# Kernel optimization log

Measured on AMD Instinct MI355X. Metric: run time of the kernel, lower is better.

The kernel has to match this reference:

```python
import jax, jax.numpy as jnp
import numpy as np

EPS = 1e-10

def setup_inputs() -> dict:
    key = jax.random.key(0)
    k1, k2 = jax.random.split(key)
    support_set = jax.random.normal(k1, (8192, 1024), dtype=jnp.float32)
    input_image = jax.random.normal(k2, (2048, 1024), dtype=jnp.float32)
    return {"support_set": support_set, "input_image": input_image}

def reference(support_set, input_image):
    # support_set: [n, d], input_image: [b, d]
    # Faithful to original: input magnitude is a single scalar over the whole
    # [b, d] input matrix; support magnitude is a scalar per support vector.
    input_mag = jax.lax.rsqrt(jnp.maximum(jnp.sum(input_image * input_image), EPS))  # scalar
    support_mag = jax.lax.rsqrt(jnp.maximum(jnp.sum(support_set * support_set, axis=1), EPS))  # [n]
    dot = jnp.einsum('bd,nd->nb', input_image, support_set)  # [n, b]
    sims = dot * support_mag[:, None] * input_mag  # [n, b]
    return sims[:, :, None]  # [n, b, 1] == torch.stack(...)[n,b,1].squeeze(1) (no-op for b>1)
```

## Files before the change

kernel.cpp:

```cpp
#include <hip/hip_runtime.h>
#include <hip/hip_bf16.h>
#include <stdint.h>
#include <stddef.h>

#define M_DIM 8192
#define N_DIM 2048
#define K_DIM 1024

#define BM 256
#define BN 256
#define BK 64
#define NKT (K_DIM / BK)
#define NITER (NKT / 2)

typedef __attribute__((ext_vector_type(8))) short short8;
typedef __attribute__((ext_vector_type(4))) float float4v;

static __device__ __forceinline__ unsigned short f2bf(float x) {
  union { float f; unsigned u; } c; c.f = x;
  return (unsigned short)((c.u + 0x7FFFu + ((c.u >> 16) & 1u)) >> 16);
}

#define GLOAD_LDS16(g, l)                                           \
  __builtin_amdgcn_global_load_lds(                                 \
      (const __attribute__((address_space(1))) void*)(g),           \
      (__attribute__((address_space(3))) void*)(l), 16, 0, 0)

__global__ __launch_bounds__(256) void prep(
    const float* __restrict__ S, const float* __restrict__ I,
    unsigned short* __restrict__ Sb, unsigned short* __restrict__ Ib,
    float* __restrict__ smag, float* __restrict__ partials) {
  const int t = threadIdx.x;
  const int lane = t & 63;
  const int wave = t >> 6;
  const int blk = blockIdx.x;
  const bool isS = blk < 2048;
  const int row = (isS ? blk : blk - 2048) * 4 + wave;
  const float* src = (isS ? S : I) + (size_t)row * K_DIM;
  unsigned short* dst = (isS ? Sb : Ib) + (size_t)row * K_DIM;

  float ss = 0.f;
#pragma unroll
  for (int i = 0; i < 4; ++i) {
    const float4 v = reinterpret_cast<const float4*>(src)[lane + i * 64];
    ushort4 b;
    b.x = f2bf(v.x); b.y = f2bf(v.y); b.z = f2bf(v.z); b.w = f2bf(v.w);
    reinterpret_cast<ushort4*>(dst)[lane + i * 64] = b;
    ss += v.x * v.x + v.y * v.y + v.z * v.z + v.w * v.w;
  }
#pragma unroll
  for (int m = 32; m >= 1; m >>= 1) ss += __shfl_xor(ss, m, 64);
  if (lane == 0) {
    if (isS) smag[row] = rsqrtf(fmaxf(ss, 1e-10f));
    else     partials[row] = ss;
  }
}

__global__ __launch_bounds__(512, 2) void gemm_bt(
    const unsigned short* __restrict__ A,
    const unsigned short* __restrict__ B,
    const float* __restrict__ smag,
    const float* __restrict__ partials,
    float* __restrict__ C) {
  __shared__ __align__(16) unsigned short lA[32768];
  __shared__ __align__(16) unsigned short lB[32768];
  __shared__ float wsum[8];

  const int t = threadIdx.x;
  const int lane = t & 63;
  const int wave = t >> 6;
  const int wr = wave >> 2;
  const int wc = wave & 3;

  const int blk = blockIdx.x;
  const int xcd = blk & 7;
  const int slot = blk >> 3;
  const int bm = (xcd * 4 + (slot & 3)) * BM;
  const int bn = (slot >> 2) * BN;

  {
    float p = partials[t] + partials[t + 512] + partials[t + 1024] + partials[t + 1536];
#pragma unroll
    for (int m = 32; m >= 1; m >>= 1) p += __shfl_xor(p, m, 64);
    if (lane == 0) wsum[wave] = p;
  }
  asm volatile("s_waitcnt vmcnt(0)" ::: "memory");

  const int srow = t >> 3;
  const int skc = (t & 7) ^ (srow & 7);
  const unsigned short* gA[4];
  const unsigned short* gB[4];
  int aoff[4];
#pragma unroll
  for (int j = 0; j < 4; ++j) {
    gA[j] = A + (size_t)(bm + j * 64 + srow) * K_DIM + skc * 8;
    gB[j] = B + (size_t)(bn + j * 64 + srow) * K_DIM + skc * 8;
    aoff[j] = (j >> 1) * 8192 + (j & 1) * 4096 + wave * 512;
  }

#define STAGE_A(j, buf) do { GLOAD_LDS16(gA[j], &lA[(buf) * 16384 + aoff[j]]); gA[j] += BK; } while (0)
#define STAGE_B(j, buf) do { GLOAD_LDS16(gB[j], &lB[(buf) * 16384 + aoff[j]]); gB[j] += BK; } while (0)
#define SP1(buf) do { STAGE_B(0, buf); STAGE_B(1, buf); } while (0)
#define SP2(buf) do { STAGE_B(2, buf); STAGE_B(3, buf); } while (0)
#define SP3(buf) do { STAGE_A(0, buf); STAGE_A(2, buf); } while (0)
#define SP4(buf) do { STAGE_A(1, buf); STAGE_A(3, buf); } while (0)

  const int fr = lane & 15;
  const int q = lane >> 4;
  const int pc0 = (q ^ (fr & 7)) * 8;
  const int pc1 = ((4 + q) ^ (fr & 7)) * 8;
  const unsigned short* rA = lA + wr * 8192 + fr * 64;
  const unsigned short* rB = lB + (wc >> 1) * 8192 + ((wc & 1) * 64 + fr) * 64;

  short8 af0[2][2], af1[2][2];
  short8 bfA[4][2], bfB[4][2];
  float4v acc[8][4];
#pragma unroll
  for (int i = 0; i < 8; ++i)
#pragma unroll
    for (int j = 0; j < 4; ++j) acc[i][j] = (float4v)0.0f;

#define BARRIER() __builtin_amdgcn_s_barrier()
#define VMW(n) asm volatile("s_waitcnt vmcnt(" #n ")" ::: "memory")
#define PRIO1() __builtin_amdgcn_s_setprio(1)
#define PRIO0() __builtin_amdgcn_s_setprio(0)

#define LOADB(bank, buf) do {                                                  \
    _Pragma("unroll") for (int nj = 0; nj < 4; ++nj) {                         \
      bank[nj][0] = *reinterpret_cast<const short8*>(rB + (buf) * 16384 + nj * 1024 + pc0); \
      bank[nj][1] = *reinterpret_cast<const short8*>(rB + (buf) * 16384 + nj * 1024 + pc1); \
    } } while (0)

#define LOADA(bank, buf, pi) do {                                              \
    _Pragma("unroll") for (int m2 = 0; m2 < 2; ++m2) {                         \
      bank[m2][0] = *reinterpret_cast<const short8*>(rA + (buf) * 16384 + ((pi) * 2 + m2) * 1024 + pc0); \
      bank[m2][1] = *reinterpret_cast<const short8*>(rA + (buf) * 16384 + ((pi) * 2 + m2) * 1024 + pc1); \
    } } while (0)

#define MFMA16(pi, abank, bbank) do {                                          \
    _Pragma("unroll") for (int m2 = 0; m2 < 2; ++m2)                           \
    _Pragma("unroll") for (int nj = 0; nj < 4; ++nj) {                         \
      acc[(pi) * 2 + m2][nj] = __builtin_amdgcn_mfma_f32_16x16x32_bf16(        \
          abank[m2][0], bbank[nj][0], acc[(pi) * 2 + m2][nj], 0, 0, 0);        \
      acc[(pi) * 2 + m2][nj] = __builtin_amdgcn_mfma_f32_16x16x32_bf16(        \
          abank[m2][1], bbank[nj][1], acc[(pi) * 2 + m2][nj], 0, 0, 0);        \
    } } while (0)

#define ITER_F() do {                                                          \
     SP4(1);           BARRIER(); LOADA(af1, 0, 1);                   \
              PRIO1(); MFMA16(0, af0, bfA); PRIO0();                           \
     SP1(0); VMW(10);  BARRIER(); LOADA(af0, 0, 2);                   \
              PRIO1(); MFMA16(1, af1, bfA); PRIO0();                           \
     SP2(0);           BARRIER(); LOADA(af1, 0, 3);                   \
              PRIO1(); MFMA16(2, af0, bfA); PRIO0();                           \
     SP3(0); VMW(8);   BARRIER(); LOADB(bfB, 1); LOADA(af0, 1, 0);    \
              PRIO1(); MFMA16(3, af1, bfA); PRIO0();                           \
     SP4(0);           BARRIER(); LOADA(af1, 1, 1);                   \
              PRIO1(); MFMA16(0, af0, bfB); PRIO0();                           \
     SP1(1); VMW(10);  BARRIER(); LOADA(af0, 1, 2);                   \
              PRIO1(); MFMA16(1, af1, bfB); PRIO0();                           \
     SP2(1);           BARRIER(); LOADA(af1, 1, 3);                   \
              PRIO1(); MFMA16(2, af0, bfB); PRIO0();                           \
     SP3(1); VMW(8);   BARRIER(); LOADB(bfA, 0); LOADA(af0, 0, 0);    \
              PRIO1(); MFMA16(3, af1, bfB); PRIO0();                           \
  } while (0)

#define ITER_T() do {                                                          \
     SP4(1);           BARRIER(); LOADA(af1, 0, 1);                   \
              PRIO1(); MFMA16(0, af0, bfA); PRIO0();                           \
     VMW(8);           BARRIER(); LOADA(af0, 0, 2);                   \
              PRIO1(); MFMA16(1, af1, bfA); PRIO0();                           \
                       BARRIER(); LOADA(af1, 0, 3);                   \
              PRIO1(); MFMA16(2, af0, bfA); PRIO0();                           \
     VMW(2);           BARRIER(); LOADB(bfB, 1); LOADA(af0, 1, 0);    \
              PRIO1(); MFMA16(3, af1, bfA); PRIO0();                           \
                       BARRIER(); LOADA(af1, 1, 1);                   \
              PRIO1(); MFMA16(0, af0, bfB); PRIO0();                           \
     VMW(0);           BARRIER(); LOADA(af0, 1, 2);                   \
              PRIO1(); MFMA16(1, af1, bfB); PRIO0();                           \
                       BARRIER(); LOADA(af1, 1, 3);                   \
              PRIO1(); MFMA16(2, af0, bfB); PRIO0();                           \
                       BARRIER();                                     \
              PRIO1(); MFMA16(3, af1, bfB); PRIO0();                           \
  } while (0)

  SP1(0); SP2(0); SP3(0); SP4(0);
  SP1(1); SP2(1); SP3(1);
  VMW(6);
  BARRIER();
  LOADB(bfA, 0); LOADA(af0, 0, 0);

#pragma unroll 1
  for (int it = 0; it < NITER - 1; ++it) ITER_F();
  ITER_T();

  const float imag = rsqrtf(fmaxf(wsum[0] + wsum[1] + wsum[2] + wsum[3] +
                                  wsum[4] + wsum[5] + wsum[6] + wsum[7], 1e-10f));
#pragma unroll
  for (int mi = 0; mi < 8; ++mi) {
    const int rbase = bm + wr * 128 + mi * 16 + q * 4;
#pragma unroll
    for (int r = 0; r < 4; ++r) {
      const int row = rbase + r;
      const float sc = smag[row] * imag;
      float* crow = C + (size_t)row * N_DIM + bn + wc * 64 + fr;
#pragma unroll
      for (int nj = 0; nj < 4; ++nj) crow[nj * 16] = acc[mi][nj][r] * sc;
    }
  }
}

extern "C" void kernel_launch(void* const* d_in, const int* in_sizes, int n_in,
                              void* d_out, int out_size, void* d_ws, size_t ws_size,
                              hipStream_t stream) {
  const float* S = (const float*)d_in[0];
  const float* I = (const float*)d_in[1];
  float* out = (float*)d_out;

  unsigned char* ws = (unsigned char*)d_ws;
  unsigned short* Sb = (unsigned short*)ws;
  unsigned short* Ib = (unsigned short*)(ws + (size_t)M_DIM * K_DIM * 2);
  float* smag = (float*)(ws + (size_t)M_DIM * K_DIM * 2 + (size_t)N_DIM * K_DIM * 2);
  float* partials = smag + M_DIM;

  hipLaunchKernelGGL(prep, dim3(2560), dim3(256), 0, stream,
                     S, I, Sb, Ib, smag, partials);
  hipLaunchKernelGGL(gemm_bt, dim3((M_DIM / BM) * (N_DIM / BN)), dim3(512), 0, stream,
                     Sb, Ib, smag, partials, out);
}
```

Measured before the change: 126.9 us.

## Restructure GEMM main loop into k-split quarter-step pipeline with nontemporal stores

```diff
diff --git a/kernel.cpp b/kernel.cpp
--- a/kernel.cpp
+++ b/kernel.cpp
@@ -112,8 +112,8 @@
   const unsigned short* rA = lA + wr * 8192 + fr * 64;
   const unsigned short* rB = lB + (wc >> 1) * 8192 + ((wc & 1) * 64 + fr) * 64;
 
-  short8 af0[2][2], af1[2][2];
-  short8 bfA[4][2], bfB[4][2];
+  short8 afA[4], afB[4];
+  short8 bf0[4], bf1[4];
   float4v acc[8][4];
 #pragma unroll
   for (int i = 0; i < 8; ++i)
@@ -125,74 +125,53 @@
 #define PRIO1() __builtin_amdgcn_s_setprio(1)
 #define PRIO0() __builtin_amdgcn_s_setprio(0)
 
-#define LOADB(bank, buf) do {                                                  \
-    _Pragma("unroll") for (int nj = 0; nj < 4; ++nj) {                         \
-      bank[nj][0] = *reinterpret_cast<const short8*>(rB + (buf) * 16384 + nj * 1024 + pc0); \
-      bank[nj][1] = *reinterpret_cast<const short8*>(rB + (buf) * 16384 + nj * 1024 + pc1); \
-    } } while (0)
-
-#define LOADA(bank, buf, pi) do {                                              \
-    _Pragma("unroll") for (int m2 = 0; m2 < 2; ++m2) {                         \
-      bank[m2][0] = *reinterpret_cast<const short8*>(rA + (buf) * 16384 + ((pi) * 2 + m2) * 1024 + pc0); \
-      bank[m2][1] = *reinterpret_cast<const short8*>(rA + (buf) * 16384 + ((pi) * 2 + m2) * 1024 + pc1); \
-    } } while (0)
-
-#define MFMA16(pi, abank, bbank) do {                                          \
-    _Pragma("unroll") for (int m2 = 0; m2 < 2; ++m2)                           \
-    _Pragma("unroll") for (int nj = 0; nj < 4; ++nj) {                         \
-      acc[(pi) * 2 + m2][nj] = __builtin_amdgcn_mfma_f32_16x16x32_bf16(        \
-          abank[m2][0], bbank[nj][0], acc[(pi) * 2 + m2][nj], 0, 0, 0);        \
-      acc[(pi) * 2 + m2][nj] = __builtin_amdgcn_mfma_f32_16x16x32_bf16(        \
-          abank[m2][1], bbank[nj][1], acc[(pi) * 2 + m2][nj], 0, 0, 0);        \
-    } } while (0)
-
-#define ITER_F() do {                                                          \
-     SP4(1);           BARRIER(); LOADA(af1, 0, 1);                   \
-              PRIO1(); MFMA16(0, af0, bfA); PRIO0();                           \
-     SP1(0); VMW(10);  BARRIER(); LOADA(af0, 0, 2);                   \
-              PRIO1(); MFMA16(1, af1, bfA); PRIO0();                           \
-     SP2(0);           BARRIER(); LOADA(af1, 0, 3);                   \
-              PRIO1(); MFMA16(2, af0, bfA); PRIO0();                           \
-     SP3(0); VMW(8);   BARRIER(); LOADB(bfB, 1); LOADA(af0, 1, 0);    \
-              PRIO1(); MFMA16(3, af1, bfA); PRIO0();                           \
-     SP4(0);           BARRIER(); LOADA(af1, 1, 1);                   \
-              PRIO1(); MFMA16(0, af0, bfB); PRIO0();                           \
-     SP1(1); VMW(10);  BARRIER(); LOADA(af0, 1, 2);                   \
-              PRIO1(); MFMA16(1, af1, bfB); PRIO0();                           \
-     SP2(1);           BARRIER(); LOADA(af1, 1, 3);                   \
-              PRIO1(); MFMA16(2, af0, bfB); PRIO0();                           \
-     SP3(1); VMW(8);   BARRIER(); LOADB(bfA, 0); LOADA(af0, 0, 0);    \
-              PRIO1(); MFMA16(3, af1, bfB); PRIO0();                           \
+#define LA(bank, buf, half, s) do {                                            \
+    _Pragma("unroll") for (int m = 0; m < 4; ++m)                              \
+      bank[m] = *reinterpret_cast<const short8*>(                              \
+          rA + (buf) * 16384 + ((half) * 4 + m) * 1024 + ((s) ? pc1 : pc0));   \
   } while (0)
 
-#define ITER_T() do {                                                          \
-     SP4(1);           BARRIER(); LOADA(af1, 0, 1);                   \
-              PRIO1(); MFMA16(0, af0, bfA); PRIO0();                           \
-     VMW(8);           BARRIER(); LOADA(af0, 0, 2);                   \
-              PRIO1(); MFMA16(1, af1, bfA); PRIO0();                           \
-                       BARRIER(); LOADA(af1, 0, 3);                   \
-              PRIO1(); MFMA16(2, af0, bfA); PRIO0();                           \
-     VMW(2);           BARRIER(); LOADB(bfB, 1); LOADA(af0, 1, 0);    \
-              PRIO1(); MFMA16(3, af1, bfA); PRIO0();                           \
-                       BARRIER(); LOADA(af1, 1, 1);                   \
-              PRIO1(); MFMA16(0, af0, bfB); PRIO0();                           \
-     VMW(0);           BARRIER(); LOADA(af0, 1, 2);                   \
-              PRIO1(); MFMA16(1, af1, bfB); PRIO0();                           \
-                       BARRIER(); LOADA(af1, 1, 3);                   \
-              PRIO1(); MFMA16(2, af0, bfB); PRIO0();                           \
-                       BARRIER();                                     \
-              PRIO1(); MFMA16(3, af1, bfB); PRIO0();                           \
+#define LB2(bank, buf, s, j0) do {                                             \
+    _Pragma("unroll") for (int n = 0; n < 2; ++n)                              \
+      bank[(j0) + n] = *reinterpret_cast<const short8*>(                       \
+          rB + (buf) * 16384 + ((j0) + n) * 1024 + ((s) ? pc1 : pc0));         \
   } while (0)
 
+#define MQ(half, abank, bbank) do {                                            \
+    PRIO1();                                                                   \
+    _Pragma("unroll") for (int m = 0; m < 4; ++m)                              \
+    _Pragma("unroll") for (int n = 0; n < 4; ++n)                              \
+      acc[(half) * 4 + m][n] = __builtin_amdgcn_mfma_f32_16x16x32_bf16(        \
+          abank[m], bbank[n], acc[(half) * 4 + m][n], 0, 0, 0);                \
+    PRIO0();                                                                   \
+  } while (0)
+
   SP1(0); SP2(0); SP3(0); SP4(0);
-  SP1(1); SP2(1); SP3(1);
-  VMW(6);
+  SP1(1);
+  VMW(2);
   BARRIER();
-  LOADB(bfA, 0); LOADA(af0, 0, 0);
+  LB2(bf0, 0, 0, 0); LB2(bf0, 0, 0, 2);
+  LA(afA, 0, 0, 0);
 
 #pragma unroll 1
-  for (int it = 0; it < NITER - 1; ++it) ITER_F();
-  ITER_T();
+  for (int it = 0; it < NITER - 1; ++it) {
+     SP2(1); VMW(4); BARRIER(); LA(afB, 0, 1, 0); LB2(bf1, 0, 1, 0); MQ(0, afA, bf0);
+     SP3(1); VMW(4); BARRIER(); LA(afA, 0, 0, 1); LB2(bf1, 0, 1, 2); MQ(1, afB, bf0);
+     SP4(1); VMW(4); BARRIER(); LA(afB, 0, 1, 1); LB2(bf0, 1, 0, 0); MQ(0, afA, bf1);
+     SP1(0); VMW(4); BARRIER(); LA(afA, 1, 0, 0); LB2(bf0, 1, 0, 2); MQ(1, afB, bf1);
+     SP2(0); VMW(4); BARRIER(); LA(afB, 1, 1, 0); LB2(bf1, 1, 1, 0); MQ(0, afA, bf0);
+     SP3(0); VMW(4); BARRIER(); LA(afA, 1, 0, 1); LB2(bf1, 1, 1, 2); MQ(1, afB, bf0);
+     SP4(0); VMW(4); BARRIER(); LA(afB, 1, 1, 1); LB2(bf0, 0, 0, 0); MQ(0, afA, bf1);
+     SP1(1); VMW(4); BARRIER(); LA(afA, 0, 0, 0); LB2(bf0, 0, 0, 2); MQ(1, afB, bf1);
+  }
+   SP2(1); VMW(4); BARRIER(); LA(afB, 0, 1, 0); LB2(bf1, 0, 1, 0); MQ(0, afA, bf0);
+   SP3(1); VMW(4); BARRIER(); LA(afA, 0, 0, 1); LB2(bf1, 0, 1, 2); MQ(1, afB, bf0);
+   SP4(1); VMW(4); BARRIER(); LA(afB, 0, 1, 1); LB2(bf0, 1, 0, 0); MQ(0, afA, bf1);
+           VMW(2); BARRIER(); LA(afA, 1, 0, 0); LB2(bf0, 1, 0, 2); MQ(1, afB, bf1);
+           VMW(0); BARRIER(); LA(afB, 1, 1, 0); LB2(bf1, 1, 1, 0); MQ(0, afA, bf0);
+                   BARRIER(); LA(afA, 1, 0, 1); LB2(bf1, 1, 1, 2); MQ(1, afB, bf0);
+                   BARRIER(); LA(afB, 1, 1, 1);                    MQ(0, afA, bf1);
+                   BARRIER();                                      MQ(1, afB, bf1);
 
   const float imag = rsqrtf(fmaxf(wsum[0] + wsum[1] + wsum[2] + wsum[3] +
                                   wsum[4] + wsum[5] + wsum[6] + wsum[7], 1e-10f));
@@ -205,7 +184,8 @@
       const float sc = smag[row] * imag;
       float* crow = C + (size_t)row * N_DIM + bn + wc * 64 + fr;
 #pragma unroll
-      for (int nj = 0; nj < 4; ++nj) crow[nj * 16] = acc[mi][nj][r] * sc;
+      for (int nj = 0; nj < 4; ++nj)
+        __builtin_nontemporal_store(acc[mi][nj][r] * sc, crow + nj * 16);
     }
   }
 }
```

After: 135.8 us. 1.07x slower.
